# Kernel optimization log

Measured on AMD Instinct MI355X. Metric: run time of the kernel, lower is better.

The kernel has to match this reference:

```python
import jax, jax.numpy as jnp
import numpy as np

RANK = 8
LORA_ALPHA = 16
SCALING = LORA_ALPHA / RANK  # 2.0
POOL, IN_DIM, OUT_DIM = 16, 2048, 2048
B, S = 16, 2048


def setup_inputs() -> dict:
    key = jax.random.key(0)
    k_x, k_idx, k_a, k_b = jax.random.split(key, 4)
    x = jax.random.normal(k_x, (B, S, IN_DIM), dtype=jnp.float32)
    idx = jax.random.randint(k_idx, (B,), 0, POOL, dtype=jnp.int64)
    # Learned params: torch inits lora_b to zeros, but we use random values so the
    # output / gradients are non-trivial for correctness testing.
    lora_a = jax.random.normal(k_a, (POOL, IN_DIM, RANK), dtype=jnp.float32)
    lora_b = jax.random.normal(k_b, (POOL, RANK, OUT_DIM), dtype=jnp.float32)
    return {"x": x, "idx": idx, "lora_a": lora_a, "lora_b": lora_b}


def reference(x, idx, lora_a, lora_b):
    # Gather per-example adapters from the pool.
    a = lora_a[idx]  # [B, IN_DIM, RANK]
    b = lora_b[idx]  # [B, RANK, OUT_DIM]
    # Mathematically identical to x @ (a @ b), but avoids the [B, IN, OUT]
    # intermediate: contract through the low rank first.
    xa = jnp.einsum('bsi,bir->bsr', x, a)       # [B, S, RANK]
    out = jnp.einsum('bsr,bro->bso', xa, b)     # [B, S, OUT_DIM]
    return out * SCALING
```

## Files before the change

kernel.cpp:

```cpp
#include <hip/hip_runtime.h>


typedef float f32x4 __attribute__((ext_vector_type(4)));

constexpr int IN_DIM  = 2048;
constexpr int OUT_DIM = 2048;
constexpr int RANK    = 8;
constexpr int S_LEN   = 2048;
constexpr int B_SZ    = 16;
constexpr int ROWS    = 4;
constexpr int SC      = 32;
constexpr int NPH     = SC / ROWS;
constexpr float SCALING = 2.0f;

__global__ __launch_bounds__(256, 2) void lora_fused_v3(
    const float* __restrict__ x,
    const int*   __restrict__ idx,
    const float* __restrict__ la,
    const float* __restrict__ lb,
    float*       __restrict__ out)
{
    const int t    = threadIdx.x;
    const int lane = t & 63;
    const int wave = t >> 6;

    constexpr int BLOCKS_PER_B = S_LEN / SC;
    const int b   = blockIdx.x / BLOCKS_PER_B;
    const int s0  = (blockIdx.x % BLOCKS_PER_B) * SC;
    const int pid = idx[b];

    float a_reg[8][RANK];
    {
        const float* ap0 = la + ((size_t)pid * IN_DIM + (size_t)t * 4) * RANK;
        const float* ap1 = ap0 + (size_t)1024 * RANK;
        #pragma unroll
        for (int j = 0; j < 4; ++j) {
            float4 v0 = *reinterpret_cast<const float4*>(ap0 + j * RANK);
            float4 v1 = *reinterpret_cast<const float4*>(ap0 + j * RANK + 4);
            a_reg[j][0]=v0.x; a_reg[j][1]=v0.y; a_reg[j][2]=v0.z; a_reg[j][3]=v0.w;
            a_reg[j][4]=v1.x; a_reg[j][5]=v1.y; a_reg[j][6]=v1.z; a_reg[j][7]=v1.w;
            float4 w0 = *reinterpret_cast<const float4*>(ap1 + j * RANK);
            float4 w1 = *reinterpret_cast<const float4*>(ap1 + j * RANK + 4);
            a_reg[4+j][0]=w0.x; a_reg[4+j][1]=w0.y; a_reg[4+j][2]=w0.z; a_reg[4+j][3]=w0.w;
            a_reg[4+j][4]=w1.x; a_reg[4+j][5]=w1.y; a_reg[4+j][6]=w1.z; a_reg[4+j][7]=w1.w;
        }
    }
    float b_reg[RANK][8];
    {
        const float* bp = lb + (size_t)pid * RANK * OUT_DIM + (size_t)t * 4;
        #pragma unroll
        for (int r = 0; r < RANK; ++r) {
            float4 v0 = *reinterpret_cast<const float4*>(bp + (size_t)r * OUT_DIM);
            float4 v1 = *reinterpret_cast<const float4*>(bp + (size_t)r * OUT_DIM + 1024);
            b_reg[r][0]=v0.x; b_reg[r][1]=v0.y; b_reg[r][2]=v0.z; b_reg[r][3]=v0.w;
            b_reg[r][4]=v1.x; b_reg[r][5]=v1.y; b_reg[r][6]=v1.z; b_reg[r][7]=v1.w;
        }
    }

    __shared__ float red[2][4][ROWS][RANK];

    const float* xbase = x   + ((size_t)b * S_LEN + s0) * IN_DIM;
    float*       obase = out + ((size_t)b * S_LEN + s0) * OUT_DIM;

    float4 xbuf[2][ROWS][2];
    #pragma unroll
    for (int row = 0; row < ROWS; ++row) {
        xbuf[0][row][0] = *reinterpret_cast<const float4*>(xbase + (size_t)row * IN_DIM + t * 4);
        xbuf[0][row][1] = *reinterpret_cast<const float4*>(xbase + (size_t)row * IN_DIM + 1024 + t * 4);
    }

    auto stage2_store = [&](int p, int rb) {
        #pragma unroll
        for (int row = 0; row < ROWS; ++row) {
            float4 lo = *reinterpret_cast<const float4*>(&red[rb][0][row][0]);
            float4 hi = *reinterpret_cast<const float4*>(&red[rb][0][row][4]);
            #pragma unroll
            for (int w = 1; w < 4; ++w) {
                float4 l2 = *reinterpret_cast<const float4*>(&red[rb][w][row][0]);
                float4 h2 = *reinterpret_cast<const float4*>(&red[rb][w][row][4]);
                lo.x += l2.x; lo.y += l2.y; lo.z += l2.z; lo.w += l2.w;
                hi.x += h2.x; hi.y += h2.y; hi.z += h2.z; hi.w += h2.w;
            }
            float xsv[RANK] = {SCALING*lo.x, SCALING*lo.y, SCALING*lo.z, SCALING*lo.w,
                               SCALING*hi.x, SCALING*hi.y, SCALING*hi.z, SCALING*hi.w};
            float ov[8];
            #pragma unroll
            for (int j = 0; j < 8; ++j) ov[j] = 0.0f;
            #pragma unroll
            for (int r = 0; r < RANK; ++r)
                #pragma unroll
                for (int j = 0; j < 8; ++j)
                    ov[j] = fmaf(xsv[r], b_reg[r][j], ov[j]);

            float* orow = obase + ((size_t)p * ROWS + row) * OUT_DIM;
            f32x4 o0 = {ov[0], ov[1], ov[2], ov[3]};
            f32x4 o1 = {ov[4], ov[5], ov[6], ov[7]};
            __builtin_nontemporal_store(o0, reinterpret_cast<f32x4*>(orow + t * 4));
            __builtin_nontemporal_store(o1, reinterpret_cast<f32x4*>(orow + 1024 + t * 4));
        }
    };

    auto phase = [&](int q, int cb) {
        if (q + 1 < NPH) {
            #pragma unroll
            for (int row = 0; row < ROWS; ++row) {
                const size_t s = (size_t)(q + 1) * ROWS + row;
                xbuf[cb ^ 1][row][0] = *reinterpret_cast<const float4*>(xbase + s * IN_DIM + t * 4);
                xbuf[cb ^ 1][row][1] = *reinterpret_cast<const float4*>(xbase + s * IN_DIM + 1024 + t * 4);
            }
        }

        float acc[ROWS][RANK];
        #pragma unroll
        for (int row = 0; row < ROWS; ++row) {
            #pragma unroll
            for (int r = 0; r < RANK; ++r) acc[row][r] = 0.0f;
            float4 xlo = xbuf[cb][row][0];
            float4 xhi = xbuf[cb][row][1];
            float xv[8] = {xlo.x, xlo.y, xlo.z, xlo.w, xhi.x, xhi.y, xhi.z, xhi.w};
            #pragma unroll
            for (int j = 0; j < 8; ++j)
                #pragma unroll
                for (int r = 0; r < RANK; ++r)
                    acc[row][r] = fmaf(xv[j], a_reg[j][r], acc[row][r]);
        }

        float m4[ROWS][4];
        {
            const bool hi = lane & 1;
            #pragma unroll
            for (int row = 0; row < ROWS; ++row)
                #pragma unroll
                for (int j = 0; j < 4; ++j) {
                    float snd = hi ? acc[row][j] : acc[row][j + 4];
                    float kp  = hi ? acc[row][j + 4] : acc[row][j];
                    m4[row][j] = kp + __shfl_xor(snd, 1);
                }
        }
        float m2[ROWS][2];
        {
            const bool hi = lane & 2;
            #pragma unroll
            for (int row = 0; row < ROWS; ++row)
                #pragma unroll
                for (int j = 0; j < 2; ++j) {
                    float snd = hi ? m4[row][j] : m4[row][j + 2];
                    float kp  = hi ? m4[row][j + 2] : m4[row][j];
                    m2[row][j] = kp + __shfl_xor(snd, 2);
                }
        }
        float m1[ROWS];
        {
            const bool hi = lane & 4;
            #pragma unroll
            for (int row = 0; row < ROWS; ++row) {
                float snd = hi ? m2[row][0] : m2[row][1];
                float kp  = hi ? m2[row][1] : m2[row][0];
                m1[row] = kp + __shfl_xor(snd, 4);
            }
        }
        float w2[2];
        {
            const bool hi = lane & 8;
            #pragma unroll
            for (int j = 0; j < 2; ++j) {
                float snd = hi ? m1[j] : m1[j + 2];
                float kp  = hi ? m1[j + 2] : m1[j];
                w2[j] = kp + __shfl_xor(snd, 8);
            }
        }
        float w1;
        {
            const bool hi = lane & 16;
            float snd = hi ? w2[0] : w2[1];
            float kp  = hi ? w2[1] : w2[0];
            w1 = kp + __shfl_xor(snd, 16);
        }
        w1 += __shfl_xor(w1, 32);

        __syncthreads();

        const int rOf   = ((lane & 1) << 2) | (lane & 2) | ((lane >> 2) & 1);
        const int rowOf = ((lane >> 2) & 2) | ((lane >> 4) & 1);
        if (lane < 32) red[cb][wave][rowOf][rOf] = w1;

        if (q >= 1) stage2_store(q - 1, cb ^ 1);
    };

    #pragma unroll
    for (int q = 0; q < NPH; q += 2) {
        phase(q, 0);
        phase(q + 1, 1);
    }

    __syncthreads();
    stage2_store(NPH - 1, (NPH - 1) & 1);
}

extern "C" void kernel_launch(void* const* d_in, const int* in_sizes, int n_in,
                              void* d_out, int out_size, void* d_ws, size_t ws_size,
                              hipStream_t stream) {
    const float* x   = (const float*)d_in[0];
    const int*   idx = (const int*)  d_in[1];
    const float* la  = (const float*)d_in[2];
    const float* lb  = (const float*)d_in[3];
    float* out = (float*)d_out;

    dim3 grid(B_SZ * (S_LEN / SC));
    lora_fused_v3<<<grid, 256, 0, stream>>>(x, idx, la, lb, out);
}
```

Before: 97.24 us.

## Split LoRA kernel into read phase and write phase with single barrier

Restructures the fused kernel so each block first computes all x·A rank-8 projections for 64 rows, processed in groups of 2 with double-buffered loads, into shared memory. A single __syncthreads follows, then B is loaded and all outputs are written. This removes the per-phase barrier and the interleaving of reads and writes, and shrinks the block count by doubling rows per block. In exchange, loads and stores no longer overlap within a block, and each block issues a long burst of stores at the end.

```diff
diff --git a/kernel.cpp b/kernel.cpp
--- a/kernel.cpp
+++ b/kernel.cpp
@@ -8,12 +8,12 @@
 constexpr int RANK    = 8;
 constexpr int S_LEN   = 2048;
 constexpr int B_SZ    = 16;
-constexpr int ROWS    = 4;
-constexpr int SC      = 32;
-constexpr int NPH     = SC / ROWS;
+constexpr int SC      = 64;
+constexpr int GR      = 2;
+constexpr int NG      = SC / GR;
 constexpr float SCALING = 2.0f;
 
-__global__ __launch_bounds__(256, 2) void lora_fused_v3(
+__global__ __launch_bounds__(256, 2) void lora_onebar(
     const float* __restrict__ x,
     const int*   __restrict__ idx,
     const float* __restrict__ la,
@@ -24,10 +24,12 @@
     const int lane = t & 63;
     const int wave = t >> 6;
 
-    constexpr int BLOCKS_PER_B = S_LEN / SC;
-    const int b   = blockIdx.x / BLOCKS_PER_B;
-    const int s0  = (blockIdx.x % BLOCKS_PER_B) * SC;
+    constexpr int BPB = S_LEN / SC;
+    const int b   = blockIdx.x / BPB;
+    const int s0  = (blockIdx.x % BPB) * SC;
     const int pid = idx[b];
+
+    __shared__ float red[SC][4][RANK];
 
     float a_reg[8][RANK];
     {
@@ -45,6 +47,96 @@
             a_reg[4+j][4]=w1.x; a_reg[4+j][5]=w1.y; a_reg[4+j][6]=w1.z; a_reg[4+j][7]=w1.w;
         }
     }
+
+    const float* xbase = x + ((size_t)b * S_LEN + s0) * IN_DIM;
+
+    float4 xbA[GR][2], xbB[GR][2];
+
+    auto load_group = [&](int g, float4 (&dst)[GR][2]) {
+        #pragma unroll
+        for (int row = 0; row < GR; ++row) {
+            const float* xr = xbase + (size_t)(g * GR + row) * IN_DIM;
+            dst[row][0] = *reinterpret_cast<const float4*>(xr + t * 4);
+            dst[row][1] = *reinterpret_cast<const float4*>(xr + 1024 + t * 4);
+        }
+    };
+
+    auto do_group = [&](int g, float4 (&cur)[GR][2], float4 (&nxt)[GR][2]) {
+        if (g + 1 < NG) load_group(g + 1, nxt);
+
+        float acc[GR][RANK];
+        #pragma unroll
+        for (int row = 0; row < GR; ++row) {
+            #pragma unroll
+            for (int r = 0; r < RANK; ++r) acc[row][r] = 0.0f;
+            float4 xlo = cur[row][0];
+            float4 xhi = cur[row][1];
+            float xv[8] = {xlo.x, xlo.y, xlo.z, xlo.w, xhi.x, xhi.y, xhi.z, xhi.w};
+            #pragma unroll
+            for (int j = 0; j < 8; ++j)
+                #pragma unroll
+                for (int r = 0; r < RANK; ++r)
+                    acc[row][r] = fmaf(xv[j], a_reg[j][r], acc[row][r]);
+        }
+
+        float m4[GR][4];
+        {
+            const bool hi = lane & 1;
+            #pragma unroll
+            for (int row = 0; row < GR; ++row)
+                #pragma unroll
+                for (int j = 0; j < 4; ++j) {
+                    float snd = hi ? acc[row][j] : acc[row][j + 4];
+                    float kp  = hi ? acc[row][j + 4] : acc[row][j];
+                    m4[row][j] = kp + __shfl_xor(snd, 1);
+                }
+        }
+        float m2[GR][2];
+        {
+            const bool hi = lane & 2;
+            #pragma unroll
+            for (int row = 0; row < GR; ++row)
+                #pragma unroll
+                for (int j = 0; j < 2; ++j) {
+                    float snd = hi ? m4[row][j] : m4[row][j + 2];
+                    float kp  = hi ? m4[row][j + 2] : m4[row][j];
+                    m2[row][j] = kp + __shfl_xor(snd, 2);
+                }
+        }
+        float m1[GR];
+        {
+            const bool hi = lane & 4;
+            #pragma unroll
+            for (int row = 0; row < GR; ++row) {
+                float snd = hi ? m2[row][0] : m2[row][1];
+                float kp  = hi ? m2[row][1] : m2[row][0];
+                m1[row] = kp + __shfl_xor(snd, 4);
+            }
+        }
+        float w1;
+        {
+            const bool hi = lane & 8;
+            float snd = hi ? m1[0] : m1[1];
+            float kp  = hi ? m1[1] : m1[0];
+            w1 = kp + __shfl_xor(snd, 8);
+        }
+        w1 += __shfl_xor(w1, 16);
+        w1 += __shfl_xor(w1, 32);
+
+        const int rOf   = ((lane & 1) << 2) | (lane & 2) | ((lane >> 2) & 1);
+        const int rowOf = (lane >> 3) & 1;
+        if (lane < 16) red[g * GR + rowOf][wave][rOf] = w1 * SCALING;
+    };
+
+    load_group(0, xbA);
+    #pragma unroll
+    for (int gg = 0; gg < NG; gg += 2) {
+        do_group(gg,     xbA, xbB);
+        do_group(gg + 1, xbB, xbA);
+    }
+
+    __syncthreads();
+
     float b_reg[RANK][8];
     {
         const float* bp = lb + (size_t)pid * RANK * OUT_DIM + (size_t)t * 4;
@@ -57,144 +149,36 @@
         }
     }
 
-    __shared__ float red[2][4][ROWS][RANK];
+    float* obase = out + ((size_t)b * S_LEN + s0) * OUT_DIM;
 
-    const float* xbase = x   + ((size_t)b * S_LEN + s0) * IN_DIM;
-    float*       obase = out + ((size_t)b * S_LEN + s0) * OUT_DIM;
+    #pragma unroll 2
+    for (int row = 0; row < SC; ++row) {
+        float4 lo = *reinterpret_cast<const float4*>(&red[row][0][0]);
+        float4 hi = *reinterpret_cast<const float4*>(&red[row][0][4]);
+        #pragma unroll
+        for (int w = 1; w < 4; ++w) {
+            float4 l2 = *reinterpret_cast<const float4*>(&red[row][w][0]);
+            float4 h2 = *reinterpret_cast<const float4*>(&red[row][w][4]);
+            lo.x += l2.x; lo.y += l2.y; lo.z += l2.z; lo.w += l2.w;
+            hi.x += h2.x; hi.y += h2.y; hi.z += h2.z; hi.w += h2.w;
+        }
+        float xs[RANK] = {lo.x, lo.y, lo.z, lo.w, hi.x, hi.y, hi.z, hi.w};
 
-    float4 xbuf[2][ROWS][2];
-    #pragma unroll
-    for (int row = 0; row < ROWS; ++row) {
-        xbuf[0][row][0] = *reinterpret_cast<const float4*>(xbase + (size_t)row * IN_DIM + t * 4);
-        xbuf[0][row][1] = *reinterpret_cast<const float4*>(xbase + (size_t)row * IN_DIM + 1024 + t * 4);
-    }
-
-    auto stage2_store = [&](int p, int rb) {
+        float ov[8];
         #pragma unroll
-        for (int row = 0; row < ROWS; ++row) {
-            float4 lo = *reinterpret_cast<const float4*>(&red[rb][0][row][0]);
-            float4 hi = *reinterpret_cast<const float4*>(&red[rb][0][row][4]);
-            #pragma unroll
-            for (int w = 1; w < 4; ++w) {
-                float4 l2 = *reinterpret_cast<const float4*>(&red[rb][w][row][0]);
-                float4 h2 = *reinterpret_cast<const float4*>(&red[rb][w][row][4]);
-                lo.x += l2.x; lo.y += l2.y; lo.z += l2.z; lo.w += l2.w;
-                hi.x += h2.x; hi.y += h2.y; hi.z += h2.z; hi.w += h2.w;
-            }
-            float xsv[RANK] = {SCALING*lo.x, SCALING*lo.y, SCALING*lo.z, SCALING*lo.w,
-                               SCALING*hi.x, SCALING*hi.y, SCALING*hi.z, SCALING*hi.w};
-            float ov[8];
-            #pragma unroll
-            for (int j = 0; j < 8; ++j) ov[j] = 0.0f;
-            #pragma unroll
-            for (int r = 0; r < RANK; ++r)
-                #pragma unroll
-                for (int j = 0; j < 8; ++j)
-                    ov[j] = fmaf(xsv[r], b_reg[r][j], ov[j]);
-
-            float* orow = obase + ((size_t)p * ROWS + row) * OUT_DIM;
-            f32x4 o0 = {ov[0], ov[1], ov[2], ov[3]};
-            f32x4 o1 = {ov[4], ov[5], ov[6], ov[7]};
-            __builtin_nontemporal_store(o0, reinterpret_cast<f32x4*>(orow + t * 4));
-            __builtin_nontemporal_store(o1, reinterpret_cast<f32x4*>(orow + 1024 + t * 4));
-        }
-    };
-
-    auto phase = [&](int q, int cb) {
-        if (q + 1 < NPH) {
-            #pragma unroll
-            for (int row = 0; row < ROWS; ++row) {
-                const size_t s = (size_t)(q + 1) * ROWS + row;
-                xbuf[cb ^ 1][row][0] = *reinterpret_cast<const float4*>(xbase + s * IN_DIM + t * 4);
-                xbuf[cb ^ 1][row][1] = *reinterpret_cast<const float4*>(xbase + s * IN_DIM + 1024 + t * 4);
-            }
-        }
-
-        float acc[ROWS][RANK];
+        for (int j = 0; j < 8; ++j) ov[j] = 0.0f;
         #pragma unroll
-        for (int row = 0; row < ROWS; ++row) {
-            #pragma unroll
-            for (int r = 0; r < RANK; ++r) acc[row][r] = 0.0f;
-            float4 xlo = xbuf[cb][row][0];
-            float4 xhi = xbuf[cb][row][1];
-            float xv[8] = {xlo.x, xlo.y, xlo.z, xlo.w, xhi.x, xhi.y, xhi.z, xhi.w};
+        for (int r = 0; r < RANK; ++r)
             #pragma unroll
             for (int j = 0; j < 8; ++j)
-                #pragma unroll
-                for (int r = 0; r < RANK; ++r)
-                    acc[row][r] = fmaf(xv[j], a_reg[j][r], acc[row][r]);
-        }
+                ov[j] = fmaf(xs[r], b_reg[r][j], ov[j]);
 
-        float m4[ROWS][4];
-        {
-            const bool hi = lane & 1;
-            #pragma unroll
-            for (int row = 0; row < ROWS; ++row)
-                #pragma unroll
-                for (int j = 0; j < 4; ++j) {
-                    float snd = hi ? acc[row][j] : acc[row][j + 4];
-                    float kp  = hi ? acc[row][j + 4] : acc[row][j];
-                    m4[row][j] = kp + __shfl_xor(snd, 1);
-                }
-        }
-        float m2[ROWS][2];
-        {
-            const bool hi = lane & 2;
-            #pragma unroll
-            for (int row = 0; row < ROWS; ++row)
-                #pragma unroll
-                for (int j = 0; j < 2; ++j) {
-                    float snd = hi ? m4[row][j] : m4[row][j + 2];
-                    float kp  = hi ? m4[row][j + 2] : m4[row][j];
-                    m2[row][j] = kp + __shfl_xor(snd, 2);
-                }
-        }
-        float m1[ROWS];
-        {
-            const bool hi = lane & 4;
-            #pragma unroll
-            for (int row = 0; row < ROWS; ++row) {
-                float snd = hi ? m2[row][0] : m2[row][1];
-                float kp  = hi ? m2[row][1] : m2[row][0];
-                m1[row] = kp + __shfl_xor(snd, 4);
-            }
-        }
-        float w2[2];
-        {
-            const bool hi = lane & 8;
-            #pragma unroll
-            for (int j = 0; j < 2; ++j) {
-                float snd = hi ? m1[j] : m1[j + 2];
-                float kp  = hi ? m1[j + 2] : m1[j];
-                w2[j] = kp + __shfl_xor(snd, 8);
-            }
-        }
-        float w1;
-        {
-            const bool hi = lane & 16;
-            float snd = hi ? w2[0] : w2[1];
-            float kp  = hi ? w2[1] : w2[0];
-            w1 = kp + __shfl_xor(snd, 16);
-        }
-        w1 += __shfl_xor(w1, 32);
-
-        __syncthreads();
-
-        const int rOf   = ((lane & 1) << 2) | (lane & 2) | ((lane >> 2) & 1);
-        const int rowOf = ((lane >> 2) & 2) | ((lane >> 4) & 1);
-        if (lane < 32) red[cb][wave][rowOf][rOf] = w1;
-
-        if (q >= 1) stage2_store(q - 1, cb ^ 1);
-    };
-
-    #pragma unroll
-    for (int q = 0; q < NPH; q += 2) {
-        phase(q, 0);
-        phase(q + 1, 1);
+        float* orow = obase + (size_t)row * OUT_DIM;
+        f32x4 o0 = {ov[0], ov[1], ov[2], ov[3]};
+        f32x4 o1 = {ov[4], ov[5], ov[6], ov[7]};
+        __builtin_nontemporal_store(o0, reinterpret_cast<f32x4*>(orow + t * 4));
+        __builtin_nontemporal_store(o1, reinterpret_cast<f32x4*>(orow + 1024 + t * 4));
     }
-
-    __syncthreads();
-    stage2_store(NPH - 1, (NPH - 1) & 1);
 }
 
 extern "C" void kernel_launch(void* const* d_in, const int* in_sizes, int n_in,
@@ -207,5 +191,5 @@
     float* out = (float*)d_out;
 
     dim3 grid(B_SZ * (S_LEN / SC));
-    lora_fused_v3<<<grid, 256, 0, stream>>>(x, idx, la, lb, out);
+    lora_onebar<<<grid, 256, 0, stream>>>(x, idx, la, lb, out);
 }
```

Measured after the change: 96.86 us. No clear change (-0.4%).
